# Performance work log

Hardware: AMD Instinct MI355X
Metric: run time of the kernel (lower is better)

The kernel has to match this reference:

```python
import jax, jax.numpy as jnp
import numpy as np

N, E, IN, OUT = 50000, 1600000, 64, 64
DIM, K = 2, 5          # pseudo-coordinate dim, kernel size per dim
KP = K ** DIM          # 25 kernel weight matrices
S = 2 ** DIM           # 4 non-zero linear B-spline basis products per edge
# bit pattern per basis product: bits[s, d] in {0,1}
_BITS = np.array([[(s >> d) & 1 for d in range(DIM)] for s in range(S)], dtype=np.int32)
_OFFS = np.array([K ** (DIM - 1 - d) for d in range(DIM)], dtype=np.int32)  # row-major flatten


def setup_inputs() -> dict:
    key = jax.random.key(0)
    ks = jax.random.split(key, 6)
    x = jax.random.normal(ks[0], (N, IN), dtype=jnp.float32)
    edge_index = jax.random.randint(ks[1], (2, E), 0, N)
    pseudo = jax.random.uniform(ks[2], (E, DIM), dtype=jnp.float32)
    bnd = 1.0 / np.sqrt(KP * IN)  # matches uniform(size) init in reset_parameters
    weight = jax.random.uniform(ks[3], (KP, IN, OUT), dtype=jnp.float32, minval=-bnd, maxval=bnd)
    root_weight = jax.random.uniform(ks[4], (IN, OUT), dtype=jnp.float32, minval=-bnd, maxval=bnd)
    bias = jax.random.uniform(ks[5], (OUT,), dtype=jnp.float32, minval=-bnd, maxval=bnd)
    return {"x": x, "edge_index": edge_index, "pseudo": pseudo,
            "weight": weight, "root_weight": root_weight, "bias": bias}


def _basis_and_index(pseudo):
    # open B-spline, degree 1: scale by (K - 1)
    v = pseudo * jnp.asarray(K - 1, pseudo.dtype)          # [E, DIM]
    lo = jnp.floor(v)
    frac = v - lo                                          # [E, DIM]
    lo = lo.astype(jnp.int32)
    bits = jnp.asarray(_BITS)                              # [S, DIM]
    # basis[e, s] = prod_d (frac if bit else 1-frac)
    terms = jnp.where(bits[None].astype(bool), frac[:, None, :], 1.0 - frac[:, None, :])
    basis = jnp.prod(terms, axis=-1)                       # [E, S]
    idx_d = (lo[:, None, :] + bits[None]) % K              # [E, S, DIM]; wrap is harmless (basis=0 there)
    idx = jnp.sum(idx_d * jnp.asarray(_OFFS), axis=-1)     # [E, S] flat weight index in [0, KP)
    return basis, idx


def reference(x, edge_index, pseudo, weight, root_weight, bias):
    row, col = edge_index[0], edge_index[1]                # row = target, col = source
    basis, idx = _basis_and_index(pseudo)                  # [E,S], [E,S]
    x_src = x[col]                                         # [E, IN] gather
    # Accumulate basis-weighted source features per (target node, kernel index),
    # then apply the dense [KP, IN, OUT] weights once (same math, no [E,IN,OUT] blowup).
    acc = jnp.zeros((N * KP, IN), x.dtype)
    for s in range(S):  # S=4, fixed structural loop
        acc = acc + jax.ops.segment_sum(basis[:, s:s + 1] * x_src,
                                        row * KP + idx[:, s], num_segments=N * KP)
    out = jnp.einsum('nki,kio->no', acc.reshape(N, KP, IN), weight)  # [N, OUT]
    deg = jax.ops.segment_sum(jnp.ones((E,), x.dtype), row, num_segments=N)
    out = out / jnp.clip(deg, 1.0)[:, None]                # mean over neighbors (1/N(i))
    return out + x @ root_weight + bias
```

## Files before the change

kernel.cpp:

```cpp
#include <hip/hip_runtime.h>
#include <hip/hip_fp16.h>
#include <hip/hip_bf16.h>


#define NN    50000
#define EE    1600000
#define NPB   16
#define KD    1664
#define ASTB  1672

#define NB    391
#define NSH   4
#define CCAP  1280
#define CSTR  16

#define REC_B 6250
#define XB_B  1563
#define WT_B  104

typedef unsigned short ushort_t;
typedef __attribute__((ext_vector_type(8))) short short8;
typedef __attribute__((ext_vector_type(4))) float f32x4;

static __device__ __forceinline__ ushort_t f2bf(float f) {
  union { float f; unsigned u; } v; v.f = f;
  return (ushort_t)((v.u + 0x7fffu + ((v.u >> 16) & 1u)) >> 16);
}
static __device__ __forceinline__ unsigned pk2bf(float a, float b) {
  __hip_bfloat162 h = __float22bfloat162_rn(make_float2(a, b));
  union { __hip_bfloat162 h; unsigned u; } cv; cv.h = h; return cv.u;
}
union S8 { short8 s; unsigned u[4]; };

__global__ __launch_bounds__(256) void k_prep(
    const int* __restrict__ ei, const float* __restrict__ pseudo,
    int* __restrict__ ccur, uint2* __restrict__ coarse,
    const float* __restrict__ x, ushort_t* __restrict__ xb,
    const float* __restrict__ w, const float* __restrict__ root,
    ushort_t* __restrict__ wt, int useXB) {
  const int b = blockIdx.x;
  const int tid = threadIdx.x;
  if (b < REC_B) {
    int e = b * 256 + tid;
    int row = ei[e], col = ei[EE + e];
    float2 pv = ((const float2*)pseudo)[e];
    float v0 = pv.x * 4.0f, v1 = pv.y * 4.0f;
    unsigned h0 = __half_as_ushort(__float2half(v0));
    unsigned h1 = __half_as_ushort(__float2half(v1));
    int c4 = (row >> 7) * NSH + (tid & (NSH - 1));
    int slot = atomicAdd(&ccur[c4 * CSTR], 1);
    if (slot < CCAP)
      coarse[(size_t)c4 * CCAP + slot] =
          make_uint2((unsigned)col | ((unsigned)(row & 127) << 16), h0 | (h1 << 16));
  } else if (b < REC_B + XB_B) {
    if (!useXB) return;
    int t = (b - REC_B) * 256 + tid;
    if (t < NN * 8) {
      const float4* xp = (const float4*)x + (size_t)t * 2;
      float4 aa = xp[0], bb = xp[1];
      S8 o;
      o.u[0] = pk2bf(aa.x, aa.y); o.u[1] = pk2bf(aa.z, aa.w);
      o.u[2] = pk2bf(bb.x, bb.y); o.u[3] = pk2bf(bb.z, bb.w);
      ((short8*)xb)[t] = o.s;
    }
  } else {
    int t = (b - REC_B - XB_B) * 256 + tid;
    int idx = t * 4;
    if (idx < 64 * KD) {
      int o = idx / KD, k = idx - o * KD;
#pragma unroll
      for (int q = 0; q < 4; ++q) {
        int kk = k + q;
        wt[idx + q] = (kk < 1600) ? f2bf(w[kk * 64 + o]) : f2bf(root[(kk - 1600) * 64 + o]);
      }
    }
  }
}

__global__ __launch_bounds__(256) void k_sort(
    const int* __restrict__ ccur, const uint2* __restrict__ coarse,
    uint2* __restrict__ recs, int* __restrict__ startA, int* __restrict__ degA) {
  __shared__ int cnt[128], lpos[128], scn[128], red[256];
  const int c = blockIdx.x, tid = threadIdx.x;
  if (tid < 128) cnt[tid] = 0;
  const int pc = c * NSH;
  int a = 0;
  for (int i = tid; i < pc; i += 256) a += min(ccur[i * CSTR], CCAP);
  red[tid] = a;
  __syncthreads();
  for (int s = 128; s > 0; s >>= 1) { if (tid < s) red[tid] += red[tid + s]; __syncthreads(); }
  const int base = red[0];
  for (int s = 0; s < NSH; ++s) {
    int n = min(ccur[(pc + s) * CSTR], CCAP);
    const uint2* seg = coarse + (size_t)(pc + s) * CCAP;
    for (int i = tid; i < n; i += 256) atomicAdd(&cnt[(seg[i].x >> 16) & 127], 1);
  }
  __syncthreads();
  if (tid < 128) scn[tid] = cnt[tid];
  __syncthreads();
  for (int ofs = 1; ofs < 128; ofs <<= 1) {
    int v = 0;
    if (tid < 128 && tid >= ofs) v = scn[tid - ofs];
    __syncthreads();
    if (tid < 128 && tid >= ofs) scn[tid] += v;
    __syncthreads();
  }
  if (tid < 128) {
    int excl = scn[tid] - cnt[tid];
    lpos[tid] = base + excl;
    int row = c * 128 + tid;
    if (row < NN) { startA[row] = base + excl; degA[row] = cnt[tid]; }
  }
  __syncthreads();
  for (int s = 0; s < NSH; ++s) {
    int n = min(ccur[(pc + s) * CSTR], CCAP);
    const uint2* seg = coarse + (size_t)(pc + s) * CCAP;
    for (int i = tid; i < n; i += 256) {
      uint2 r = seg[i];
      int dst = atomicAdd(&lpos[(r.x >> 16) & 127], 1);
      recs[dst] = make_uint2(r.x & 0xFFFFu, r.y);
    }
  }
}

template <bool XBF>
__global__ __launch_bounds__(1024, 4) void k_main(
    const uint2* __restrict__ recs, const int* __restrict__ startA,
    const int* __restrict__ degA,
    const float* __restrict__ x, const ushort_t* __restrict__ xb,
    const ushort_t* __restrict__ wt, const float* __restrict__ bias,
    float* __restrict__ out) {
  __shared__ ushort_t accS[NPB * ASTB];
  __shared__ float    outp[4 * NPB * 64];
  __shared__ float    sinv[NPB];
  const int tid = threadIdx.x;
  const int lane = tid & 63;
  const int w = tid >> 6;
  const int node = blockIdx.x * NPB + w;

  const int m = degA[node];
  const float dcf = (float)max(m, 1);
  if (lane == 0) sinv[w] = 1.0f / dcf;
  accS[w * ASTB + 1600 + lane] = f2bf(x[(size_t)node * 64 + lane] * dcf);

  const int m15 = lane & 15, quad = lane >> 4;
  const float r0f = (float)(m15 / 5),        c0f = (float)(m15 % 5);
  const float r1f = (float)((16 + m15) / 5), c1f = (float)((16 + m15) % 5);

  f32x4 acc[2][4];
#pragma unroll
  for (int a = 0; a < 2; ++a)
#pragma unroll
    for (int b = 0; b < 4; ++b) acc[a][b] = (f32x4){0.f, 0.f, 0.f, 0.f};

  const uint2* bket = recs + startA[node];
  unsigned rcx = 0u, rcy = 0x7C007C00u;
  if (lane < m) { uint2 rr = bket[lane]; rcx = rr.x; rcy = rr.y; }

  for (int e0 = 0; e0 < m; e0 += 32) {
    if (e0 && !(e0 & 63)) {
      rcx = 0u; rcy = 0x7C007C00u;
      int idx = e0 + lane;
      if (idx < m) { uint2 rr = bket[idx]; rcx = rr.x; rcy = rr.y; }
    }
    const int eb = (e0 & 32) + quad * 8;
    unsigned cj[8], pj[8];
#pragma unroll
    for (int j = 0; j < 8; ++j) {
      cj[j] = (unsigned)__shfl((int)rcx, eb + j);
      pj[j] = (unsigned)__shfl((int)rcy, eb + j);
    }
    unsigned gv[4][8];
    float    gf[4][8];
#pragma unroll
    for (int j = 0; j < 8; ++j) {
      if (XBF) {
        const ushort_t* xr = xb + (size_t)cj[j] * 64 + m15;
        gv[0][j] = xr[0]; gv[1][j] = xr[16]; gv[2][j] = xr[32]; gv[3][j] = xr[48];
      } else {
        const float* xr = x + (size_t)cj[j] * 64 + m15;
        gf[0][j] = xr[0]; gf[1][j] = xr[16]; gf[2][j] = xr[32]; gf[3][j] = xr[48];
      }
    }
    S8 aT0, aT1, bT[4];
#pragma unroll
    for (int p = 0; p < 4; ++p) {
      float a0[2], a1[2];
#pragma unroll
      for (int q = 0; q < 2; ++q) {
        unsigned pv = pj[2 * p + q];
        float v0 = __half2float(__ushort_as_half((ushort_t)(pv & 0xFFFFu)));
        float v1 = __half2float(__ushort_as_half((ushort_t)(pv >> 16)));
        a0[q] = fmaxf(0.f, 1.f - fabsf(v0 - r0f)) * fmaxf(0.f, 1.f - fabsf(v1 - c0f));
        a1[q] = fmaxf(0.f, 1.f - fabsf(v0 - r1f)) * fmaxf(0.f, 1.f - fabsf(v1 - c1f));
      }
      aT0.u[p] = pk2bf(a0[0], a0[1]);
      aT1.u[p] = pk2bf(a1[0], a1[1]);
    }
#pragma unroll
    for (int p = 0; p < 4; ++p)
#pragma unroll
      for (int t = 0; t < 4; ++t)
        bT[t].u[p] = XBF ? (gv[t][2 * p] | (gv[t][2 * p + 1] << 16))
                         : pk2bf(gf[t][2 * p], gf[t][2 * p + 1]);
    __builtin_amdgcn_s_setprio(1);
#pragma unroll
    for (int t = 0; t < 4; ++t) {
      acc[0][t] = __builtin_amdgcn_mfma_f32_16x16x32_bf16(aT0.s, bT[t].s, acc[0][t], 0, 0, 0);
      acc[1][t] = __builtin_amdgcn_mfma_f32_16x16x32_bf16(aT1.s, bT[t].s, acc[1][t], 0, 0, 0);
    }
    __builtin_amdgcn_s_setprio(0);
  }

#pragma unroll
  for (int mt = 0; mt < 2; ++mt)
#pragma unroll
    for (int r = 0; r < 4; ++r) {
      int kp = mt * 16 + quad * 4 + r;
      if (kp < 25) {
#pragma unroll
        for (int nt = 0; nt < 4; ++nt)
          accS[w * ASTB + kp * 64 + nt * 16 + m15] = f2bf(acc[mt][nt][r]);
      }
    }
  __syncthreads();

  {
    const int ntile = w & 3, kh = w >> 2;
    const int m2 = lane & 15, quad2 = lane >> 4;
    const int nn2 = ntile * 16 + m2;
    f32x4 d = {0.0f, 0.0f, 0.0f, 0.0f};
    const ushort_t* ab = &accS[m2 * ASTB + kh * 416 + quad2 * 8];
    const ushort_t* wb = &wt[(size_t)nn2 * KD + kh * 416 + quad2 * 8];
    for (int kk = 0; kk < 13; ++kk) {
      short8 af = *(const short8*)(ab + kk * 32);
      short8 bf = *(const short8*)(wb + kk * 32);
      d = __builtin_amdgcn_mfma_f32_16x16x32_bf16(af, bf, d, 0, 0, 0);
    }
#pragma unroll
    for (int r = 0; r < 4; ++r)
      outp[kh * (NPB * 64) + (quad2 * 4 + r) * 64 + ntile * 16 + m2] = d[r];
  }
  __syncthreads();

  {
    float conv = outp[0 * (NPB * 64) + w * 64 + lane]
               + outp[1 * (NPB * 64) + w * 64 + lane]
               + outp[2 * (NPB * 64) + w * 64 + lane]
               + outp[3 * (NPB * 64) + w * 64 + lane];
    out[(size_t)node * 64 + lane] = conv * sinv[w] + bias[lane];
  }
}

__global__ void k_sentinel(float* __restrict__ out) {
  int i = blockIdx.x * 256 + threadIdx.x;
  if (i < NN * 64) out[i] = 1000.0f;
}

extern "C" void kernel_launch(void* const* d_in, const int* in_sizes, int n_in,
                              void* d_out, int out_size, void* d_ws, size_t ws_size,
                              hipStream_t stream) {
  const float* x      = (const float*)d_in[0];
  const int*   ei     = (const int*)d_in[1];
  const float* pseudo = (const float*)d_in[2];
  const float* w      = (const float*)d_in[3];
  const float* root   = (const float*)d_in[4];
  const float* bias   = (const float*)d_in[5];
  float* out = (float*)d_out;
  (void)in_sizes; (void)n_in; (void)out_size;

  char* ws = (char*)d_ws;
  size_t off = 0;
  auto alloc = [&](size_t bytes) { size_t r = off; off += (bytes + 511) & ~(size_t)511; return r; };
  ushort_t* wt     = (ushort_t*)(ws + alloc((size_t)64 * KD * 2));
  int*      ccur   = (int*)(ws + alloc((size_t)NB * NSH * CSTR * 4));
  int*      startA = (int*)(ws + alloc((size_t)NN * 4));
  int*      degA   = (int*)(ws + alloc((size_t)NN * 4));
  uint2*    recs   = (uint2*)(ws + alloc((size_t)EE * 8));
  uint2*    coarse = (uint2*)(ws + alloc((size_t)NB * NSH * CCAP * 8));
  size_t baseNeed  = off;
  ushort_t* xb     = (ushort_t*)(ws + alloc((size_t)NN * 64 * 2));
  size_t fullNeed  = off;

  if (ws_size < baseNeed) {
    k_sentinel<<<(NN * 64 + 255) / 256, 256, 0, stream>>>(out);
    return;
  }
  const int useXB = (ws_size >= fullNeed) ? 1 : 0;

  hipMemsetAsync(ccur, 0, (size_t)NB * NSH * CSTR * 4, stream);
  k_prep<<<REC_B + XB_B + WT_B, 256, 0, stream>>>(ei, pseudo, ccur, coarse,
                                                  x, xb, w, root, wt, useXB);
  k_sort<<<NB, 256, 0, stream>>>(ccur, coarse, recs, startA, degA);
  if (useXB)
    k_main<true><<<NN / NPB, 1024, 0, stream>>>(recs, startA, degA, x, xb, wt, bias, out);
  else
    k_main<false><<<NN / NPB, 1024, 0, stream>>>(recs, startA, degA, x, xb, wt, bias, out);
}
```

Baseline: 325.7 us.

## Load edge records directly per quad and issue gathers via inline asm

The per-wave edge-record load plus cross-lane shuffles is replaced by each quad reading its 8 records straight from memory, with the first two 32-edge chunks prefetched up front. The bf16 source-feature gather is now hand-written global_load_ushort asm with a single explicit vmcnt wait placed after the basis computation, so the basis math overlaps the outstanding gathers. Out-of-range edges are masked by zeroing basis weights and clamping the source index. This removes shuffle overhead and exposed gather latency, but it reads records past the node's bucket end and relies on the asm wait ordering being correct.

```diff
diff --git a/kernel.cpp b/kernel.cpp
--- a/kernel.cpp
+++ b/kernel.cpp
@@ -123,6 +123,127 @@
   }
 }
 
+static __device__ __forceinline__ void gather32(
+    const ushort_t* __restrict__ xb, const unsigned* vo, unsigned (&g)[4][8]) {
+  asm volatile(
+      "global_load_ushort %[g00], %[a0], %[sb]\n\t"
+      "global_load_ushort %[g10], %[a0], %[sb] offset:32\n\t"
+      "global_load_ushort %[g20], %[a0], %[sb] offset:64\n\t"
+      "global_load_ushort %[g30], %[a0], %[sb] offset:96\n\t"
+      "global_load_ushort %[g01], %[a1], %[sb]\n\t"
+      "global_load_ushort %[g11], %[a1], %[sb] offset:32\n\t"
+      "global_load_ushort %[g21], %[a1], %[sb] offset:64\n\t"
+      "global_load_ushort %[g31], %[a1], %[sb] offset:96\n\t"
+      "global_load_ushort %[g02], %[a2], %[sb]\n\t"
+      "global_load_ushort %[g12], %[a2], %[sb] offset:32\n\t"
+      "global_load_ushort %[g22], %[a2], %[sb] offset:64\n\t"
+      "global_load_ushort %[g32], %[a2], %[sb] offset:96\n\t"
+      "global_load_ushort %[g03], %[a3], %[sb]\n\t"
+      "global_load_ushort %[g13], %[a3], %[sb] offset:32\n\t"
+      "global_load_ushort %[g23], %[a3], %[sb] offset:64\n\t"
+      "global_load_ushort %[g33], %[a3], %[sb] offset:96\n\t"
+      : [g00] "=&v"(g[0][0]), [g10] "=&v"(g[1][0]), [g20] "=&v"(g[2][0]), [g30] "=&v"(g[3][0]),
+        [g01] "=&v"(g[0][1]), [g11] "=&v"(g[1][1]), [g21] "=&v"(g[2][1]), [g31] "=&v"(g[3][1]),
+        [g02] "=&v"(g[0][2]), [g12] "=&v"(g[1][2]), [g22] "=&v"(g[2][2]), [g32] "=&v"(g[3][2]),
+        [g03] "=&v"(g[0][3]), [g13] "=&v"(g[1][3]), [g23] "=&v"(g[2][3]), [g33] "=&v"(g[3][3])
+      : [a0] "v"(vo[0]), [a1] "v"(vo[1]), [a2] "v"(vo[2]), [a3] "v"(vo[3]), [sb] "s"(xb));
+  asm volatile(
+      "global_load_ushort %[g04], %[a4], %[sb]\n\t"
+      "global_load_ushort %[g14], %[a4], %[sb] offset:32\n\t"
+      "global_load_ushort %[g24], %[a4], %[sb] offset:64\n\t"
+      "global_load_ushort %[g34], %[a4], %[sb] offset:96\n\t"
+      "global_load_ushort %[g05], %[a5], %[sb]\n\t"
+      "global_load_ushort %[g15], %[a5], %[sb] offset:32\n\t"
+      "global_load_ushort %[g25], %[a5], %[sb] offset:64\n\t"
+      "global_load_ushort %[g35], %[a5], %[sb] offset:96\n\t"
+      "global_load_ushort %[g06], %[a6], %[sb]\n\t"
+      "global_load_ushort %[g16], %[a6], %[sb] offset:32\n\t"
+      "global_load_ushort %[g26], %[a6], %[sb] offset:64\n\t"
+      "global_load_ushort %[g36], %[a6], %[sb] offset:96\n\t"
+      "global_load_ushort %[g07], %[a7], %[sb]\n\t"
+      "global_load_ushort %[g17], %[a7], %[sb] offset:32\n\t"
+      "global_load_ushort %[g27], %[a7], %[sb] offset:64\n\t"
+      "global_load_ushort %[g37], %[a7], %[sb] offset:96\n\t"
+      : [g04] "=&v"(g[0][4]), [g14] "=&v"(g[1][4]), [g24] "=&v"(g[2][4]), [g34] "=&v"(g[3][4]),
+        [g05] "=&v"(g[0][5]), [g15] "=&v"(g[1][5]), [g25] "=&v"(g[2][5]), [g35] "=&v"(g[3][5]),
+        [g06] "=&v"(g[0][6]), [g16] "=&v"(g[1][6]), [g26] "=&v"(g[2][6]), [g36] "=&v"(g[3][6]),
+        [g07] "=&v"(g[0][7]), [g17] "=&v"(g[1][7]), [g27] "=&v"(g[2][7]), [g37] "=&v"(g[3][7])
+      : [a4] "v"(vo[4]), [a5] "v"(vo[5]), [a6] "v"(vo[6]), [a7] "v"(vo[7]), [sb] "s"(xb));
+}
+static __device__ __forceinline__ void gather32_wait(unsigned (&g)[4][8]) {
+  asm volatile("s_waitcnt vmcnt(0)"
+               : "+v"(g[0][0]), "+v"(g[1][0]), "+v"(g[2][0]), "+v"(g[3][0]),
+                 "+v"(g[0][1]), "+v"(g[1][1]), "+v"(g[2][1]), "+v"(g[3][1]),
+                 "+v"(g[0][2]), "+v"(g[1][2]), "+v"(g[2][2]), "+v"(g[3][2]),
+                 "+v"(g[0][3]), "+v"(g[1][3]), "+v"(g[2][3]), "+v"(g[3][3]));
+  asm volatile(""
+               : "+v"(g[0][4]), "+v"(g[1][4]), "+v"(g[2][4]), "+v"(g[3][4]),
+                 "+v"(g[0][5]), "+v"(g[1][5]), "+v"(g[2][5]), "+v"(g[3][5]),
+                 "+v"(g[0][6]), "+v"(g[1][6]), "+v"(g[2][6]), "+v"(g[3][6]),
+                 "+v"(g[0][7]), "+v"(g[1][7]), "+v"(g[2][7]), "+v"(g[3][7]));
+}
+
+template <bool XBF>
+static __device__ __forceinline__ void do_chunk(
+    const uint2 (&rq)[8], int kb, int m, int quad, int m15,
+    float r0f, float c0f, float r1f, float c1f,
+    const ushort_t* __restrict__ xb, const float* __restrict__ x,
+    f32x4 (&acc)[2][4]) {
+  unsigned cj[8], pj[8];
+#pragma unroll
+  for (int j = 0; j < 8; ++j) {
+    cj[j] = min(rq[j].x, 49999u);
+    pj[j] = rq[j].y;
+  }
+  unsigned g[4][8];
+  float gf[4][8];
+  if (XBF) {
+    unsigned vo[8];
+#pragma unroll
+    for (int j = 0; j < 8; ++j) vo[j] = (cj[j] << 7) + (unsigned)(m15 << 1);
+    gather32(xb, vo, g);
+  } else {
+#pragma unroll
+    for (int j = 0; j < 8; ++j) {
+      const float* xr = x + (size_t)cj[j] * 64 + m15;
+      gf[0][j] = xr[0]; gf[1][j] = xr[16]; gf[2][j] = xr[32]; gf[3][j] = xr[48];
+    }
+  }
+  S8 aT0, aT1, bT[4];
+#pragma unroll
+  for (int p = 0; p < 4; ++p) {
+    float a0[2], a1[2];
+#pragma unroll
+    for (int q = 0; q < 2; ++q) {
+      int j = 2 * p + q;
+      unsigned pv = pj[j];
+      float v0 = __half2float(__ushort_as_half((ushort_t)(pv & 0xFFFFu)));
+      float v1 = __half2float(__ushort_as_half((ushort_t)(pv >> 16)));
+      bool ok = (kb + quad * 8 + j) < m;
+      float p0 = fmaxf(0.f, 1.f - fabsf(v0 - r0f)) * fmaxf(0.f, 1.f - fabsf(v1 - c0f));
+      float p1 = fmaxf(0.f, 1.f - fabsf(v0 - r1f)) * fmaxf(0.f, 1.f - fabsf(v1 - c1f));
+      a0[q] = ok ? p0 : 0.0f;
+      a1[q] = ok ? p1 : 0.0f;
+    }
+    aT0.u[p] = pk2bf(a0[0], a0[1]);
+    aT1.u[p] = pk2bf(a1[0], a1[1]);
+  }
+  if (XBF) gather32_wait(g);
+#pragma unroll
+  for (int p = 0; p < 4; ++p)
+#pragma unroll
+    for (int t = 0; t < 4; ++t)
+      bT[t].u[p] = XBF ? (g[t][2 * p] | (g[t][2 * p + 1] << 16))
+                       : pk2bf(gf[t][2 * p], gf[t][2 * p + 1]);
+  __builtin_amdgcn_s_setprio(1);
+#pragma unroll
+  for (int t = 0; t < 4; ++t) {
+    acc[0][t] = __builtin_amdgcn_mfma_f32_16x16x32_bf16(aT0.s, bT[t].s, acc[0][t], 0, 0, 0);
+    acc[1][t] = __builtin_amdgcn_mfma_f32_16x16x32_bf16(aT1.s, bT[t].s, acc[1][t], 0, 0, 0);
+  }
+  __builtin_amdgcn_s_setprio(0);
+}
+
 template <bool XBF>
 __global__ __launch_bounds__(1024, 4) void k_main(
     const uint2* __restrict__ recs, const int* __restrict__ startA,
@@ -154,62 +275,21 @@
     for (int b = 0; b < 4; ++b) acc[a][b] = (f32x4){0.f, 0.f, 0.f, 0.f};
 
   const uint2* bket = recs + startA[node];
-  unsigned rcx = 0u, rcy = 0x7C007C00u;
-  if (lane < m) { uint2 rr = bket[lane]; rcx = rr.x; rcy = rr.y; }
-
-  for (int e0 = 0; e0 < m; e0 += 32) {
-    if (e0 && !(e0 & 63)) {
-      rcx = 0u; rcy = 0x7C007C00u;
-      int idx = e0 + lane;
-      if (idx < m) { uint2 rr = bket[idx]; rcx = rr.x; rcy = rr.y; }
-    }
-    const int eb = (e0 & 32) + quad * 8;
-    unsigned cj[8], pj[8];
-#pragma unroll
-    for (int j = 0; j < 8; ++j) {
-      cj[j] = (unsigned)__shfl((int)rcx, eb + j);
-      pj[j] = (unsigned)__shfl((int)rcy, eb + j);
-    }
-    unsigned gv[4][8];
-    float    gf[4][8];
-#pragma unroll
-    for (int j = 0; j < 8; ++j) {
-      if (XBF) {
-        const ushort_t* xr = xb + (size_t)cj[j] * 64 + m15;
-        gv[0][j] = xr[0]; gv[1][j] = xr[16]; gv[2][j] = xr[32]; gv[3][j] = xr[48];
-      } else {
-        const float* xr = x + (size_t)cj[j] * 64 + m15;
-        gf[0][j] = xr[0]; gf[1][j] = xr[16]; gf[2][j] = xr[32]; gf[3][j] = xr[48];
-      }
-    }
-    S8 aT0, aT1, bT[4];
-#pragma unroll
-    for (int p = 0; p < 4; ++p) {
-      float a0[2], a1[2];
-#pragma unroll
-      for (int q = 0; q < 2; ++q) {
-        unsigned pv = pj[2 * p + q];
-        float v0 = __half2float(__ushort_as_half((ushort_t)(pv & 0xFFFFu)));
-        float v1 = __half2float(__ushort_as_half((ushort_t)(pv >> 16)));
-        a0[q] = fmaxf(0.f, 1.f - fabsf(v0 - r0f)) * fmaxf(0.f, 1.f - fabsf(v1 - c0f));
-        a1[q] = fmaxf(0.f, 1.f - fabsf(v0 - r1f)) * fmaxf(0.f, 1.f - fabsf(v1 - c1f));
-      }
-      aT0.u[p] = pk2bf(a0[0], a0[1]);
-      aT1.u[p] = pk2bf(a1[0], a1[1]);
-    }
-#pragma unroll
-    for (int p = 0; p < 4; ++p)
-#pragma unroll
-      for (int t = 0; t < 4; ++t)
-        bT[t].u[p] = XBF ? (gv[t][2 * p] | (gv[t][2 * p + 1] << 16))
-                         : pk2bf(gf[t][2 * p], gf[t][2 * p + 1]);
-    __builtin_amdgcn_s_setprio(1);
-#pragma unroll
-    for (int t = 0; t < 4; ++t) {
-      acc[0][t] = __builtin_amdgcn_mfma_f32_16x16x32_bf16(aT0.s, bT[t].s, acc[0][t], 0, 0, 0);
-      acc[1][t] = __builtin_amdgcn_mfma_f32_16x16x32_bf16(aT1.s, bT[t].s, acc[1][t], 0, 0, 0);
-    }
-    __builtin_amdgcn_s_setprio(0);
+  uint2 rq0[8], rq1[8];
+#pragma unroll
+  for (int j = 0; j < 8; ++j) {
+    rq0[j] = bket[quad * 8 + j];
+    rq1[j] = bket[32 + quad * 8 + j];
+  }
+  if (m > 0)
+    do_chunk<XBF>(rq0, 0, m, quad, m15, r0f, c0f, r1f, c1f, xb, x, acc);
+  if (m > 32)
+    do_chunk<XBF>(rq1, 32, m, quad, m15, r0f, c0f, r1f, c1f, xb, x, acc);
+  for (int e0 = 64; e0 < m; e0 += 32) {
+    uint2 rqx[8];
+#pragma unroll
+    for (int j = 0; j < 8; ++j) rqx[j] = bket[e0 + quad * 8 + j];
+    do_chunk<XBF>(rqx, e0, m, quad, m15, r0f, c0f, r1f, c1f, xb, x, acc);
   }
 
 #pragma unroll
```

Result: slower. 341.4 us (+4.8%).

## Process two nodes per wave with 512-thread blocks and direct record loads

Applied to the files above, without the earlier changes.

The main kernel moves from 1024-thread blocks with one node per wave to 512-thread blocks where each wave handles two nodes in sequence. Edge records are now loaded per lane directly instead of through wave shuffles, and validity is handled by masking the basis weights. The final weight GEMM splits K two ways instead of four and keeps a rotating prefetch of weight fragments in registers. Start and degree are packed into one uint2 array. The changes cut the shuffle and partial-sum overhead, at the cost of fewer waves to hide gather latency and more serial work per wave.

```diff
diff --git a/kernel.cpp b/kernel.cpp
--- a/kernel.cpp
+++ b/kernel.cpp
@@ -79,7 +79,7 @@
 
 __global__ __launch_bounds__(256) void k_sort(
     const int* __restrict__ ccur, const uint2* __restrict__ coarse,
-    uint2* __restrict__ recs, int* __restrict__ startA, int* __restrict__ degA) {
+    uint2* __restrict__ recs, uint2* __restrict__ nfo) {
   __shared__ int cnt[128], lpos[128], scn[128], red[256];
   const int c = blockIdx.x, tid = threadIdx.x;
   if (tid < 128) cnt[tid] = 0;
@@ -109,7 +109,7 @@
     int excl = scn[tid] - cnt[tid];
     lpos[tid] = base + excl;
     int row = c * 128 + tid;
-    if (row < NN) { startA[row] = base + excl; degA[row] = cnt[tid]; }
+    if (row < NN) nfo[row] = make_uint2((unsigned)(base + excl), (unsigned)cnt[tid]);
   }
   __syncthreads();
   for (int s = 0; s < NSH; ++s) {
@@ -124,105 +124,120 @@
 }
 
 template <bool XBF>
-__global__ __launch_bounds__(1024, 4) void k_main(
-    const uint2* __restrict__ recs, const int* __restrict__ startA,
-    const int* __restrict__ degA,
+static __device__ __forceinline__ void do_chunk(
+    const uint2 (&rq)[8], int kb, int m, int quad, int m15,
+    float r0f, float c0f, float r1f, float c1f,
+    const ushort_t* __restrict__ xb, const float* __restrict__ x,
+    f32x4 (&acc)[2][4]) {
+  unsigned cj[8], pj[8];
+#pragma unroll
+  for (int j = 0; j < 8; ++j) {
+    cj[j] = min(rq[j].x, (unsigned)(NN - 1));
+    pj[j] = rq[j].y;
+  }
+  unsigned g[4][8];
+  float gf[4][8];
+  if (XBF) {
+#pragma unroll
+    for (int j = 0; j < 8; ++j) {
+      const ushort_t* xr = xb + ((size_t)cj[j] << 6) + m15;
+      g[0][j] = xr[0]; g[1][j] = xr[16]; g[2][j] = xr[32]; g[3][j] = xr[48];
+    }
+  } else {
+#pragma unroll
+    for (int j = 0; j < 8; ++j) {
+      const float* xr = x + ((size_t)cj[j] << 6) + m15;
+      gf[0][j] = xr[0]; gf[1][j] = xr[16]; gf[2][j] = xr[32]; gf[3][j] = xr[48];
+    }
+  }
+  S8 aT0, aT1, bT[4];
+#pragma unroll
+  for (int p = 0; p < 4; ++p) {
+    float a0[2], a1[2];
+#pragma unroll
+    for (int q = 0; q < 2; ++q) {
+      int j = 2 * p + q;
+      unsigned pv = pj[j];
+      float v0 = __half2float(__ushort_as_half((ushort_t)(pv & 0xFFFFu)));
+      float v1 = __half2float(__ushort_as_half((ushort_t)(pv >> 16)));
+      bool ok = (kb + quad * 8 + j) < m;
+      float p0 = fmaxf(0.f, 1.f - fabsf(v0 - r0f)) * fmaxf(0.f, 1.f - fabsf(v1 - c0f));
+      float p1 = fmaxf(0.f, 1.f - fabsf(v0 - r1f)) * fmaxf(0.f, 1.f - fabsf(v1 - c1f));
+      a0[q] = ok ? p0 : 0.0f;
+      a1[q] = ok ? p1 : 0.0f;
+    }
+    aT0.u[p] = pk2bf(a0[0], a0[1]);
+    aT1.u[p] = pk2bf(a1[0], a1[1]);
+  }
+#pragma unroll
+  for (int p = 0; p < 4; ++p)
+#pragma unroll
+    for (int t = 0; t < 4; ++t)
+      bT[t].u[p] = XBF ? (g[t][2 * p] | (g[t][2 * p + 1] << 16))
+                       : pk2bf(gf[t][2 * p], gf[t][2 * p + 1]);
+  __builtin_amdgcn_s_setprio(1);
+#pragma unroll
+  for (int t = 0; t < 4; ++t) {
+    acc[0][t] = __builtin_amdgcn_mfma_f32_16x16x32_bf16(aT0.s, bT[t].s, acc[0][t], 0, 0, 0);
+    acc[1][t] = __builtin_amdgcn_mfma_f32_16x16x32_bf16(aT1.s, bT[t].s, acc[1][t], 0, 0, 0);
+  }
+  __builtin_amdgcn_s_setprio(0);
+}
+
+template <bool XBF>
+__global__ __launch_bounds__(512, 4) void k_main(
+    const uint2* __restrict__ recs, const uint2* __restrict__ nfo,
     const float* __restrict__ x, const ushort_t* __restrict__ xb,
     const ushort_t* __restrict__ wt, const float* __restrict__ bias,
     float* __restrict__ out) {
   __shared__ ushort_t accS[NPB * ASTB];
-  __shared__ float    outp[4 * NPB * 64];
+  __shared__ float    outp[2 * NPB * 64];
   __shared__ float    sinv[NPB];
   const int tid = threadIdx.x;
   const int lane = tid & 63;
   const int w = tid >> 6;
-  const int node = blockIdx.x * NPB + w;
-
-  const int m = degA[node];
-  const float dcf = (float)max(m, 1);
-  if (lane == 0) sinv[w] = 1.0f / dcf;
-  accS[w * ASTB + 1600 + lane] = f2bf(x[(size_t)node * 64 + lane] * dcf);
+  const int nb = blockIdx.x * NPB;
 
   const int m15 = lane & 15, quad = lane >> 4;
   const float r0f = (float)(m15 / 5),        c0f = (float)(m15 % 5);
   const float r1f = (float)((16 + m15) / 5), c1f = (float)((16 + m15) % 5);
 
-  f32x4 acc[2][4];
-#pragma unroll
-  for (int a = 0; a < 2; ++a)
-#pragma unroll
-    for (int b = 0; b < 4; ++b) acc[a][b] = (f32x4){0.f, 0.f, 0.f, 0.f};
-
-  const uint2* bket = recs + startA[node];
-  unsigned rcx = 0u, rcy = 0x7C007C00u;
-  if (lane < m) { uint2 rr = bket[lane]; rcx = rr.x; rcy = rr.y; }
-
-  for (int e0 = 0; e0 < m; e0 += 32) {
-    if (e0 && !(e0 & 63)) {
-      rcx = 0u; rcy = 0x7C007C00u;
-      int idx = e0 + lane;
-      if (idx < m) { uint2 rr = bket[idx]; rcx = rr.x; rcy = rr.y; }
-    }
-    const int eb = (e0 & 32) + quad * 8;
-    unsigned cj[8], pj[8];
-#pragma unroll
-    for (int j = 0; j < 8; ++j) {
-      cj[j] = (unsigned)__shfl((int)rcx, eb + j);
-      pj[j] = (unsigned)__shfl((int)rcy, eb + j);
-    }
-    unsigned gv[4][8];
-    float    gf[4][8];
-#pragma unroll
-    for (int j = 0; j < 8; ++j) {
-      if (XBF) {
-        const ushort_t* xr = xb + (size_t)cj[j] * 64 + m15;
-        gv[0][j] = xr[0]; gv[1][j] = xr[16]; gv[2][j] = xr[32]; gv[3][j] = xr[48];
-      } else {
-        const float* xr = x + (size_t)cj[j] * 64 + m15;
-        gf[0][j] = xr[0]; gf[1][j] = xr[16]; gf[2][j] = xr[32]; gf[3][j] = xr[48];
+#pragma unroll
+  for (int nd = 0; nd < 2; ++nd) {
+    const int row = (w << 1) + nd;
+    const int node = nb + row;
+    const uint2 nf = nfo[node];
+    const int m = (int)nf.y;
+    const float dcf = (float)max(m, 1);
+    if (lane == 0) sinv[row] = 1.0f / dcf;
+    accS[row * ASTB + 1600 + lane] = f2bf(x[(size_t)node * 64 + lane] * dcf);
+
+    f32x4 acc[2][4];
+#pragma unroll
+    for (int a = 0; a < 2; ++a)
+#pragma unroll
+      for (int b = 0; b < 4; ++b) acc[a][b] = (f32x4){0.f, 0.f, 0.f, 0.f};
+
+    const uint2* bket = recs + nf.x;
+    for (int e0 = 0; e0 < m; e0 += 32) {
+      uint2 rq[8];
+#pragma unroll
+      for (int j = 0; j < 8; ++j) rq[j] = bket[e0 + quad * 8 + j];
+      do_chunk<XBF>(rq, e0, m, quad, m15, r0f, c0f, r1f, c1f, xb, x, acc);
+    }
+
+#pragma unroll
+    for (int mt = 0; mt < 2; ++mt)
+#pragma unroll
+      for (int r = 0; r < 4; ++r) {
+        int kp = mt * 16 + quad * 4 + r;
+        if (kp < 25) {
+#pragma unroll
+          for (int nt = 0; nt < 4; ++nt)
+            accS[row * ASTB + kp * 64 + nt * 16 + m15] = f2bf(acc[mt][nt][r]);
+        }
       }
-    }
-    S8 aT0, aT1, bT[4];
-#pragma unroll
-    for (int p = 0; p < 4; ++p) {
-      float a0[2], a1[2];
-#pragma unroll
-      for (int q = 0; q < 2; ++q) {
-        unsigned pv = pj[2 * p + q];
-        float v0 = __half2float(__ushort_as_half((ushort_t)(pv & 0xFFFFu)));
-        float v1 = __half2float(__ushort_as_half((ushort_t)(pv >> 16)));
-        a0[q] = fmaxf(0.f, 1.f - fabsf(v0 - r0f)) * fmaxf(0.f, 1.f - fabsf(v1 - c0f));
-        a1[q] = fmaxf(0.f, 1.f - fabsf(v0 - r1f)) * fmaxf(0.f, 1.f - fabsf(v1 - c1f));
-      }
-      aT0.u[p] = pk2bf(a0[0], a0[1]);
-      aT1.u[p] = pk2bf(a1[0], a1[1]);
-    }
-#pragma unroll
-    for (int p = 0; p < 4; ++p)
-#pragma unroll
-      for (int t = 0; t < 4; ++t)
-        bT[t].u[p] = XBF ? (gv[t][2 * p] | (gv[t][2 * p + 1] << 16))
-                         : pk2bf(gf[t][2 * p], gf[t][2 * p + 1]);
-    __builtin_amdgcn_s_setprio(1);
-#pragma unroll
-    for (int t = 0; t < 4; ++t) {
-      acc[0][t] = __builtin_amdgcn_mfma_f32_16x16x32_bf16(aT0.s, bT[t].s, acc[0][t], 0, 0, 0);
-      acc[1][t] = __builtin_amdgcn_mfma_f32_16x16x32_bf16(aT1.s, bT[t].s, acc[1][t], 0, 0, 0);
-    }
-    __builtin_amdgcn_s_setprio(0);
-  }
-
-#pragma unroll
-  for (int mt = 0; mt < 2; ++mt)
-#pragma unroll
-    for (int r = 0; r < 4; ++r) {
-      int kp = mt * 16 + quad * 4 + r;
-      if (kp < 25) {
-#pragma unroll
-        for (int nt = 0; nt < 4; ++nt)
-          accS[w * ASTB + kp * 64 + nt * 16 + m15] = f2bf(acc[mt][nt][r]);
-      }
-    }
+  }
   __syncthreads();
 
   {
@@ -230,12 +245,16 @@
     const int m2 = lane & 15, quad2 = lane >> 4;
     const int nn2 = ntile * 16 + m2;
     f32x4 d = {0.0f, 0.0f, 0.0f, 0.0f};
-    const ushort_t* ab = &accS[m2 * ASTB + kh * 416 + quad2 * 8];
-    const ushort_t* wb = &wt[(size_t)nn2 * KD + kh * 416 + quad2 * 8];
-    for (int kk = 0; kk < 13; ++kk) {
+    const ushort_t* ab = &accS[m2 * ASTB + kh * 832 + quad2 * 8];
+    const ushort_t* wb = &wt[(size_t)nn2 * KD + kh * 832 + quad2 * 8];
+    short8 bfs[6];
+#pragma unroll
+    for (int kk = 0; kk < 6; ++kk) bfs[kk] = *(const short8*)(wb + kk * 32);
+#pragma unroll
+    for (int kk = 0; kk < 26; ++kk) {
       short8 af = *(const short8*)(ab + kk * 32);
-      short8 bf = *(const short8*)(wb + kk * 32);
-      d = __builtin_amdgcn_mfma_f32_16x16x32_bf16(af, bf, d, 0, 0, 0);
+      d = __builtin_amdgcn_mfma_f32_16x16x32_bf16(af, bfs[kk % 6], d, 0, 0, 0);
+      if (kk + 6 < 26) bfs[kk % 6] = *(const short8*)(wb + (kk + 6) * 32);
     }
 #pragma unroll
     for (int r = 0; r < 4; ++r)
@@ -244,11 +263,13 @@
   __syncthreads();
 
   {
-    float conv = outp[0 * (NPB * 64) + w * 64 + lane]
-               + outp[1 * (NPB * 64) + w * 64 + lane]
-               + outp[2 * (NPB * 64) + w * 64 + lane]
-               + outp[3 * (NPB * 64) + w * 64 + lane];
-    out[(size_t)node * 64 + lane] = conv * sinv[w] + bias[lane];
+#pragma unroll
+    for (int h = 0; h < 2; ++h) {
+      int i = h * 512 + tid;
+      int nl = i >> 6, o = i & 63;
+      float conv = outp[i] + outp[NPB * 64 + i];
+      out[(size_t)(nb + nl) * 64 + o] = conv * sinv[nl] + bias[o];
+    }
   }
 }
 
@@ -274,8 +295,7 @@
   auto alloc = [&](size_t bytes) { size_t r = off; off += (bytes + 511) & ~(size_t)511; return r; };
   ushort_t* wt     = (ushort_t*)(ws + alloc((size_t)64 * KD * 2));
   int*      ccur   = (int*)(ws + alloc((size_t)NB * NSH * CSTR * 4));
-  int*      startA = (int*)(ws + alloc((size_t)NN * 4));
-  int*      degA   = (int*)(ws + alloc((size_t)NN * 4));
+  uint2*    nfo    = (uint2*)(ws + alloc((size_t)NN * 8));
   uint2*    recs   = (uint2*)(ws + alloc((size_t)EE * 8));
   uint2*    coarse = (uint2*)(ws + alloc((size_t)NB * NSH * CCAP * 8));
   size_t baseNeed  = off;
@@ -291,9 +311,9 @@
   hipMemsetAsync(ccur, 0, (size_t)NB * NSH * CSTR * 4, stream);
   k_prep<<<REC_B + XB_B + WT_B, 256, 0, stream>>>(ei, pseudo, ccur, coarse,
                                                   x, xb, w, root, wt, useXB);
-  k_sort<<<NB, 256, 0, stream>>>(ccur, coarse, recs, startA, degA);
+  k_sort<<<NB, 256, 0, stream>>>(ccur, coarse, recs, nfo);
   if (useXB)
-    k_main<true><<<NN / NPB, 1024, 0, stream>>>(recs, startA, degA, x, xb, wt, bias, out);
+    k_main<true><<<NN / NPB, 512, 0, stream>>>(recs, nfo, x, xb, wt, bias, out);
   else
-    k_main<false><<<NN / NPB, 1024, 0, stream>>>(recs, startA, degA, x, xb, wt, bias, out);
-}
+    k_main<false><<<NN / NPB, 512, 0, stream>>>(recs, nfo, x, xb, wt, bias, out);
+}
```

New measurement: 316.4 us. -2.9%, faster.
